# Kernel tuning notes

Measured on AMD Instinct MI355X. Metric: run time of the kernel, lower is better.

## Reference

```python
import jax, jax.numpy as jnp
import numpy as np

N_ROWS = 8_388_608  # candidate rows
N_VARS = 8          # variable_end


def setup_inputs() -> dict:
    key = jax.random.key(0)
    inputs = jax.random.normal(key, (N_ROWS, N_VARS), dtype=jnp.float32)
    return {"inputs": inputs}


def reference(inputs):
    # Expression tree (prefix seq [11,8,9,8,9,0,1,12,2,13,15,14,3,10,4,8,9,5,5,13,6,7]):
    # tanh( (x0*x1 + sin(x2)) * exp(-|x3|) + x4 / (x5*x5 + exp(x6)) - x7 )
    x0, x1, x2, x3 = inputs[:, 0], inputs[:, 1], inputs[:, 2], inputs[:, 3]
    x4, x5, x6, x7 = inputs[:, 4], inputs[:, 5], inputs[:, 6], inputs[:, 7]
    expr = (x0 * x1 + jnp.sin(x2)) * jnp.exp(-jnp.abs(x3)) \
        + x4 / (x5 * x5 + jnp.exp(x6)) - x7
    return jnp.tanh(expr)
```

## Files before the change

### kernel.cpp

```cpp
#include <hip/hip_runtime.h>
#include <hip/hip_bf16.h>
#include <math.h>


__device__ __forceinline__ float fast_rcp(float x) {
    return __builtin_amdgcn_rcpf(x);
}

__device__ __forceinline__ float fast_tanh(float x) {
    float a = fabsf(x);
    float e = __expf(-2.0f * a);
    float r = fast_rcp(1.0f + e);
    float t = __builtin_fmaf(-(e + e), r, 1.0f);
    return copysignf(t, x);
}

__global__ __launch_bounds__(256) void Expression_82643760709953_kernel(
    const float4* __restrict__ in4, float* __restrict__ out, int n_rows) {
    int idx = blockIdx.x * blockDim.x + threadIdx.x;
    int stride = gridDim.x * blockDim.x;
    for (int i = idx; i < n_rows; i += stride) {
        float4 a = in4[2 * i];
        float4 b = in4[2 * i + 1];
        float s  = __sinf(a.z);
        float e3 = __expf(-fabsf(a.w));
        float t1 = __builtin_fmaf(a.x, a.y, s) * e3;
        float den = __builtin_fmaf(b.y, b.y, __expf(b.z));
        float t2 = b.x * fast_rcp(den);
        float expr = t1 + t2 - b.w;
        out[i] = fast_tanh(expr);
    }
}

extern "C" void kernel_launch(void* const* d_in, const int* in_sizes, int n_in,
                              void* d_out, int out_size, void* d_ws, size_t ws_size,
                              hipStream_t stream) {
    const float4* in4 = (const float4*)d_in[0];
    float* out = (float*)d_out;
    int n_rows = out_size;
    int block = 256;
    int grid = (n_rows + block - 1) / block;
    Expression_82643760709953_kernel<<<grid, block, 0, stream>>>(in4, out, n_rows);
}
```

Baseline: 353.5 us.

## Process four rows per thread with nontemporal loads and a capped grid-stride loop

Each thread now handles four consecutive rows, issuing eight 16-byte nontemporal loads and one vectorized 16-byte nontemporal store. The grid is capped at 2048 blocks and uses a grid-stride loop, with a scalar tail loop for leftover rows. The intent is more bytes in flight per thread, fewer store instructions, and less cache pollution for a streaming, bandwidth-bound kernel. The trade-off is that each load instruction's lanes are now spread over a wider address range (128 bytes apart per lane), which may hurt coalescing.

```diff
diff --git a/kernel.cpp b/kernel.cpp
--- a/kernel.cpp
+++ b/kernel.cpp
@@ -1,7 +1,8 @@
 #include <hip/hip_runtime.h>
-#include <hip/hip_bf16.h>
 #include <math.h>
 
+
+typedef float v4f __attribute__((ext_vector_type(4)));
 
 __device__ __forceinline__ float fast_rcp(float x) {
     return __builtin_amdgcn_rcpf(x);
@@ -15,30 +16,58 @@
     return copysignf(t, x);
 }
 
+__device__ __forceinline__ float row_expr(v4f a, v4f b) {
+    float s   = __sinf(a[2]);
+    float e3  = __expf(-fabsf(a[3]));
+    float t1  = __builtin_fmaf(a[0], a[1], s) * e3;
+    float den = __builtin_fmaf(b[1], b[1], __expf(b[2]));
+    float t2  = b[0] * fast_rcp(den);
+    return fast_tanh(t1 + t2 - b[3]);
+}
+
 __global__ __launch_bounds__(256) void Expression_82643760709953_kernel(
-    const float4* __restrict__ in4, float* __restrict__ out, int n_rows) {
-    int idx = blockIdx.x * blockDim.x + threadIdx.x;
-    int stride = gridDim.x * blockDim.x;
-    for (int i = idx; i < n_rows; i += stride) {
-        float4 a = in4[2 * i];
-        float4 b = in4[2 * i + 1];
-        float s  = __sinf(a.z);
-        float e3 = __expf(-fabsf(a.w));
-        float t1 = __builtin_fmaf(a.x, a.y, s) * e3;
-        float den = __builtin_fmaf(b.y, b.y, __expf(b.z));
-        float t2 = b.x * fast_rcp(den);
-        float expr = t1 + t2 - b.w;
-        out[i] = fast_tanh(expr);
+    const v4f* __restrict__ in4, float* __restrict__ out, int n_rows) {
+    const int tid = blockIdx.x * blockDim.x + threadIdx.x;
+    const int nth = gridDim.x * blockDim.x;
+    const int stride = 4 * nth;
+
+    int r = 4 * tid;
+    for (; r + 3 < n_rows; r += stride) {
+        const v4f* p = &in4[2 * r];
+        v4f a0 = __builtin_nontemporal_load(&p[0]);
+        v4f b0 = __builtin_nontemporal_load(&p[1]);
+        v4f a1 = __builtin_nontemporal_load(&p[2]);
+        v4f b1 = __builtin_nontemporal_load(&p[3]);
+        v4f a2 = __builtin_nontemporal_load(&p[4]);
+        v4f b2 = __builtin_nontemporal_load(&p[5]);
+        v4f a3 = __builtin_nontemporal_load(&p[6]);
+        v4f b3 = __builtin_nontemporal_load(&p[7]);
+        v4f o;
+        o[0] = row_expr(a0, b0);
+        o[1] = row_expr(a1, b1);
+        o[2] = row_expr(a2, b2);
+        o[3] = row_expr(a3, b3);
+        __builtin_nontemporal_store(o, (v4f*)&out[r]);
+    }
+    if (r < n_rows) {
+        for (int t = r; t < n_rows; ++t) {
+            v4f a = __builtin_nontemporal_load(&in4[2 * t]);
+            v4f b = __builtin_nontemporal_load(&in4[2 * t + 1]);
+            out[t] = row_expr(a, b);
+        }
     }
 }
 
 extern "C" void kernel_launch(void* const* d_in, const int* in_sizes, int n_in,
                               void* d_out, int out_size, void* d_ws, size_t ws_size,
                               hipStream_t stream) {
-    const float4* in4 = (const float4*)d_in[0];
+    const v4f* in4 = (const v4f*)d_in[0];
     float* out = (float*)d_out;
     int n_rows = out_size;
     int block = 256;
-    int grid = (n_rows + block - 1) / block;
+    long quads = ((long)n_rows + 3) / 4;
+    long need = (quads + block - 1) / block;
+    int grid = (int)(need < 2048 ? need : 2048);
+    if (grid < 1) grid = 1;
     Expression_82643760709953_kernel<<<grid, block, 0, stream>>>(in4, out, n_rows);
 }
```

After: 404.8 us. 1.15x slower.
